# Kernel tuning notes

Hardware: AMD Instinct MI355X
Metric: run time of the kernel (lower is better)

Reference implementation:

```python
import jax, jax.numpy as jnp
import numpy as np

MAX_REL = 16  # max_relative_position (keys == values)


def _relative_positions(T, max_pos):
    r = jnp.arange(T)
    dist = r[None, :] - r[:, None]          # [T, T], k - q
    return jnp.clip(dist, -max_pos, max_pos) + max_pos


def setup_inputs() -> dict:
    key = jax.random.key(0)
    ks = jax.random.split(key, 5)
    B, H, T, D = 4, 16, 1024, 64
    V = 2 * MAX_REL + 1
    return {
        "q": jax.random.normal(ks[0], (B, H, T, D), jnp.float32),
        "k": jax.random.normal(ks[1], (B, H, T, D), jnp.float32),
        "v": jax.random.normal(ks[2], (B, H, T, D), jnp.float32),
        "emb_k": jax.random.normal(ks[3], (V, D), jnp.float32),
        "emb_v": jax.random.normal(ks[4], (V, D), jnp.float32),
    }


def reference(q, k, v, emb_k, emb_v):
    # q,k,v: [B,H,T,D]; emb_*: [2*MAX_REL+1, D]
    T = q.shape[2]
    D = k.shape[-1]
    rel_idx = _relative_positions(T, MAX_REL)          # [T,T]
    rel_k = emb_k[rel_idx]                             # [T,T,D]
    rel_v = emb_v[rel_idx]                             # [T,T,D]

    # content-content + content-position logits
    logits = jnp.einsum('bhtd,bhsd->bhts', q, k)
    logits = logits + jnp.einsum('bhtd,tsd->bhts', q, rel_k)
    logits = logits * (1.0 / jnp.sqrt(jnp.float32(D)))

    attn = jax.nn.softmax(logits, axis=-1)             # [B,H,T,T]
    out = jnp.einsum('bhts,bhsd->bhtd', attn, v)
    out = out + jnp.einsum('bhts,tsd->bhtd', attn, rel_v)
    return out, attn
```

## Files before the change

kernel.cpp:

```cpp
#include <hip/hip_runtime.h>
#include <hip/hip_bf16.h>

#define TT 1024
#define DD 64
#define MAXREL 16
#define NV 33
#define QBLK 16
#define SCALE 0.125f
#define BH 64

typedef short bf16x8 __attribute__((ext_vector_type(8)));
typedef short bf16x4 __attribute__((ext_vector_type(4)));
typedef float f32x4 __attribute__((ext_vector_type(4)));

#define SBAR() __builtin_amdgcn_sched_barrier(0)
#define WAITV(N)   __builtin_amdgcn_s_waitcnt(0x0F70 | (N))
#define WAITLGKM() __builtin_amdgcn_s_waitcnt(0xC07F)

static __device__ inline void gload16(const void* g, void* l) {
    __builtin_amdgcn_global_load_lds(
        (const __attribute__((address_space(1))) void*)g,
        (__attribute__((address_space(3))) void*)l, 16, 0, 0);
}

static __device__ inline short f2bf(float f) {
    __hip_bfloat16 h = __float2bfloat16(f);
    return *(short*)&h;
}
static __device__ inline float bf2f(short s) {
    union { unsigned u; float f; } x;
    x.u = ((unsigned)(unsigned short)s) << 16;
    return x.f;
}
static __device__ inline bf16x8 pack8(float4 a, float4 b) {
    bf16x8 r;
    r[0]=f2bf(a.x); r[1]=f2bf(a.y); r[2]=f2bf(a.z); r[3]=f2bf(a.w);
    r[4]=f2bf(b.x); r[5]=f2bf(b.y); r[6]=f2bf(b.z); r[7]=f2bf(b.w);
    return r;
}

__global__ __launch_bounds__(256)
void prep_kernel(const float* __restrict__ k, const float* __restrict__ v,
                 short* __restrict__ kbuf, short* __restrict__ vt) {
    __shared__ short tile[64][66];
    const int bh = blockIdx.x >> 4;
    const int s0 = (blockIdx.x & 15) * 64;
    const int t  = threadIdx.x;
    const int r  = t >> 2;
    const int g  = t & 3;

    {
        const float* kp = k + ((size_t)bh * TT + s0 + r) * DD + g * 16;
        float4 a0 = *(const float4*)(kp);
        float4 a1 = *(const float4*)(kp + 4);
        float4 a2 = *(const float4*)(kp + 8);
        float4 a3 = *(const float4*)(kp + 12);
        short* dp = kbuf + ((size_t)bh * TT + s0 + r) * DD + g * 16;
        *(bf16x8*)dp       = pack8(a0, a1);
        *(bf16x8*)(dp + 8) = pack8(a2, a3);
    }
    {
        const float* vp = v + ((size_t)bh * TT + s0 + r) * DD + g * 16;
        float4 a0 = *(const float4*)(vp);
        float4 a1 = *(const float4*)(vp + 4);
        float4 a2 = *(const float4*)(vp + 8);
        float4 a3 = *(const float4*)(vp + 12);
        bf16x8 b0 = pack8(a0, a1), b1 = pack8(a2, a3);
        #pragma unroll
        for (int j = 0; j < 8; ++j) {
            tile[g * 16 + j][r]     = b0[j];
            tile[g * 16 + 8 + j][r] = b1[j];
        }
    }
    __syncthreads();
    {
        const int d = t >> 2, c = t & 3;
        bf16x8 o0 = *(const bf16x8*)&tile[d][c * 16];
        bf16x8 o1 = *(const bf16x8*)&tile[d][c * 16 + 8];
        short* dp = vt + ((size_t)bh * DD + d) * TT + s0 + c * 16;
        *(bf16x8*)dp       = o0;
        *(bf16x8*)(dp + 8) = o1;
    }
}

__global__ __launch_bounds__(512)
void relattn_kernel(const float* __restrict__ q_g,
                    const short* __restrict__ kb,
                    const short* __restrict__ vt,
                    const float* __restrict__ ek_g,
                    const float* __restrict__ ev_g,
                    float* __restrict__ out_g,
                    float* __restrict__ attn_g) {
    __shared__ __align__(16) char pbuf[QBLK * 2048];
    __shared__ __align__(16) char kstage[8 * 4096];
    __shared__ float pair_lds[4][16][16];
    __shared__ float qe_lds[QBLK * NV];
    __shared__ float w_lds[QBLK * NV];
    __shared__ float psum_lds[QBLK][8];
    __shared__ float psuf_lds[QBLK][8];
    __shared__ float pmid_lds[QBLK][8];
    __shared__ float inv_lds[QBLK];

    const int t    = threadIdx.x;
    const int bid  = blockIdx.x;
    const int wg   = ((bid & 7) << 9) | (bid >> 3);
    const int bh   = wg >> 6;
    const int q0   = (wg & 63) * QBLK;
    const int w    = t >> 6;
    const int lane = t & 63;
    const int lr   = lane & 15;
    const int akg  = lane >> 4;
    const int srl  = lane >> 3;
    const int sqg  = (lane & 7) ^ srl;

    const short* kgbase = kb + (size_t)bh * TT * DD;
    char* kst = kstage + w * 4096;

    auto KSTAGE = [&](int B, int NT) {
        const int s0 = w * 128 + NT * 16;
        gload16(kgbase + (size_t)(s0 + srl) * 64 + sqg * 8,     kst + B * 2048);
        gload16(kgbase + (size_t)(s0 + 8 + srl) * 64 + sqg * 8, kst + B * 2048 + 1024);
    };

    bf16x8 qF0, qF1;
    {
        const float* qp = q_g + ((size_t)bh * TT + q0 + lr) * DD + akg * 8;
        float4 a = *(const float4*)qp,        b = *(const float4*)(qp + 4);
        float4 c = *(const float4*)(qp + 32), d = *(const float4*)(qp + 36);
        qF0 = pack8(a, b); qF1 = pack8(c, d);
    }

    KSTAGE(0, 0); KSTAGE(1, 1);

    for (int i = t; i < QBLK * NV; i += 512) w_lds[i] = 0.f;
    if (w < 3) {
        int v = w * 16 + lr; if (v > 32) v = 32;
        const float* ep = ek_g + v * DD + akg * 8;
        float4 a = *(const float4*)ep,        b = *(const float4*)(ep + 4);
        float4 c = *(const float4*)(ep + 32), d = *(const float4*)(ep + 36);
        bf16x8 eF0 = pack8(a, b), eF1 = pack8(c, d);
        f32x4 qacc = {0.f, 0.f, 0.f, 0.f};
        qacc = __builtin_amdgcn_mfma_f32_16x16x32_bf16(eF0, qF0, qacc, 0, 0, 0);
        qacc = __builtin_amdgcn_mfma_f32_16x16x32_bf16(eF1, qF1, qacc, 0, 0, 0);
        #pragma unroll
        for (int j = 0; j < 4; ++j) {
            int vv = w * 16 + akg * 4 + j;
            if (vv < NV) qe_lds[lr * NV + vv] = __expf(qacc[j] * SCALE);
        }
    }
    __syncthreads();

    {
        const int tq = q0 + lr;
        const int X  = (lr & 7) << 4;
        const float eqe_lo = qe_lds[lr * NV];
        const float eqe_hi = qe_lds[lr * NV + 32];
        float sum = 0.f, suff = 0.f, msum = 0.f;

        auto CVALU = [&](f32x4 acc, int nt) {
            const int sb = w * 128 + nt * 16 + akg * 4;
            float ex0 = __expf(acc[0] * SCALE), ex1 = __expf(acc[1] * SCALE);
            float ex2 = __expf(acc[2] * SCALE), ex3 = __expf(acc[3] * SCALE);
            float e0, e1, e2, e3;
            if (sb >= tq + MAXREL) {
                e0 = ex0 * eqe_hi; e1 = ex1 * eqe_hi;
                e2 = ex2 * eqe_hi; e3 = ex3 * eqe_hi;
                float csum = (e0 + e1) + (e2 + e3);
                sum += csum; suff += csum;
            } else if (sb + 3 <= tq - MAXREL) {
                e0 = ex0 * eqe_lo; e1 = ex1 * eqe_lo;
                e2 = ex2 * eqe_lo; e3 = ex3 * eqe_lo;
                sum += (e0 + e1) + (e2 + e3);
            } else {
                float ee[4]; float exs[4] = {ex0, ex1, ex2, ex3};
                #pragma unroll
                for (int j = 0; j < 4; ++j) {
                    int dr = sb + j - tq;
                    int dc = dr < -MAXREL ? -MAXREL : (dr > MAXREL ? MAXREL : dr);
                    float v = exs[j] * qe_lds[lr * NV + dc + MAXREL];
                    ee[j] = v;
                    sum += v;
                    if (dr >= MAXREL) suff += v;
                    if (dr > -MAXREL && dr < MAXREL) {
                        w_lds[lr * NV + dr + MAXREL] = v;
                        msum += v;
                    }
                }
                e0 = ee[0]; e1 = ee[1]; e2 = ee[2]; e3 = ee[3];
            }
            bf16x4 p4;
            p4[0] = f2bf(e0); p4[1] = f2bf(e1);
            p4[2] = f2bf(e2); p4[3] = f2bf(e3);
            *(bf16x4*)(pbuf + lr * 2048 + ((2 * sb) ^ X)) = p4;
        };

        auto MFMA2 = [&](bf16x8 kf0, bf16x8 kf1) {
            f32x4 acc = {0.f, 0.f, 0.f, 0.f};
            acc = __builtin_amdgcn_mfma_f32_16x16x32_bf16(kf0, qF0, acc, 0, 0, 0);
            acc = __builtin_amdgcn_mfma_f32_16x16x32_bf16(kf1, qF1, acc, 0, 0, 0);
            return acc;
        };

        f32x4 aA, aB;
        #define CITER(B, NT, W, PF, AC, AP, NP) \
            WAITV(W); SBAR(); \
            { bf16x8 kf0 = *(const bf16x8*)(kst + (B)*2048 + lr*128 + ((((akg))  ^(lr&7)) << 4)); \
              bf16x8 kf1 = *(const bf16x8*)(kst + (B)*2048 + lr*128 + ((((akg)+4)^(lr&7)) << 4)); \
              if ((NP) >= 0) CVALU(AP, NP); \
              WAITLGKM(); SBAR(); \
              if (PF) KSTAGE((B), (NT) + 2); \
              AC = MFMA2(kf0, kf1); } \
            SBAR()
        CITER(0, 0, 2, 1, aA, aB, -1);
        CITER(1, 1, 2, 1, aB, aA,  0);
        CITER(0, 2, 2, 1, aA, aB,  1);
        CITER(1, 3, 2, 1, aB, aA,  2);
        CITER(0, 4, 2, 1, aA, aB,  3);
        CITER(1, 5, 2, 1, aB, aA,  4);
        CITER(0, 6, 2, 0, aA, aB,  5);
        CITER(1, 7, 0, 0, aB, aA,  6);
        CVALU(aB, 7);
        #undef CITER

        {
            WAITLGKM(); SBAR();
            const short* vgbase = vt + ((size_t)bh * DD + (w & 3) * 16) * TT;
            const int S0 = (w >> 2) * 8;
            gload16(vgbase + (size_t)srl * TT + S0 * 64 + sqg * 8,           kst);
            gload16(vgbase + (size_t)(8 + srl) * TT + S0 * 64 + sqg * 8,     kst + 1024);
            gload16(vgbase + (size_t)srl * TT + (S0 + 1) * 64 + sqg * 8,     kst + 2048);
            gload16(vgbase + (size_t)(8 + srl) * TT + (S0 + 1) * 64 + sqg * 8, kst + 3072);
        }

        sum  += __shfl_xor(sum, 16);  sum  += __shfl_xor(sum, 32);
        suff += __shfl_xor(suff, 16); suff += __shfl_xor(suff, 32);
        msum += __shfl_xor(msum, 16); msum += __shfl_xor(msum, 32);
        if (lane < 16) {
            psum_lds[lr][w] = sum;
            psuf_lds[lr][w] = suff;
            pmid_lds[lr][w] = msum;
        }
    }
    __syncthreads();

    if (t < QBLK) {
        float s = 0.f, sf = 0.f, sm = 0.f;
        #pragma unroll
        for (int i = 0; i < 8; ++i) {
            s  += psum_lds[t][i];
            sf += psuf_lds[t][i];
            sm += pmid_lds[t][i];
        }
        inv_lds[t] = 1.0f / s;
        w_lds[t * NV]      = s - sf - sm;
        w_lds[t * NV + 32] = sf;
    }
    __syncthreads();

    {
        const int dt = w & 3;
        const int sh = w >> 2;
        const int S0 = sh * 8;
        const int lc = lane & 15;
        const int dcol = dt * 16 + lc;
        const char* pb = pbuf + lc * 2048;
        const int X = (lc & 7) << 4;
        char* vst = kst;
        const short* vgbase = vt + ((size_t)bh * DD + dt * 16) * TT;
        float* ab = attn_g + ((size_t)bh * TT + q0) * TT;
        f32x4 acc0 = {0.f, 0.f, 0.f, 0.f};
        f32x4 acc1 = {0.f, 0.f, 0.f, 0.f};

        auto VSTAGE = [&](int B, int S) {
            gload16(vgbase + (size_t)srl * TT + S * 64 + sqg * 8,       vst + B * 2048);
            gload16(vgbase + (size_t)(8 + srl) * TT + S * 64 + sqg * 8, vst + B * 2048 + 1024);
        };

        auto ASTORE = [&](int ST) {
            const int r_ = w * 2 + (ST >> 2);
            const int i_ = ST & 3;
            const float inv_ = inv_lds[r_];
            const int Xr = (r_ & 7) << 4;
            bf16x4 p4 = *(const bf16x4*)(pbuf + r_ * 2048 + ((8 * lane + 512 * i_) ^ Xr));
            f32x4 o;
            o[0] = bf2f(p4[0]) * inv_; o[1] = bf2f(p4[1]) * inv_;
            o[2] = bf2f(p4[2]) * inv_; o[3] = bf2f(p4[3]) * inv_;
            __builtin_nontemporal_store(o, (f32x4*)(ab + (size_t)r_ * TT + lane * 4 + 256 * i_));
        };

        #define FITER(B, S, W, PF, AC, ST) \
            WAITV(W); SBAR(); \
            { ASTORE(ST); \
              bf16x8 vf0 = *(const bf16x8*)(vst + (B)*2048 + lc*128 + ((((akg))  ^(lc&7)) << 4)); \
              bf16x8 vf1 = *(const bf16x8*)(vst + (B)*2048 + lc*128 + ((((akg)+4)^(lc&7)) << 4)); \
              bf16x8 a0 = *(const bf16x8*)(pb + (((2*(S))*64     + akg*16) ^ X)); \
              bf16x8 a1 = *(const bf16x8*)(pb + (((2*(S)+1)*64   + akg*16) ^ X)); \
              WAITLGKM(); SBAR(); \
              if (PF) VSTAGE((B), (S) + 2); \
              AC = __builtin_amdgcn_mfma_f32_16x16x32_bf16(a0, vf0, AC, 0, 0, 0); \
              AC = __builtin_amdgcn_mfma_f32_16x16x32_bf16(a1, vf1, AC, 0, 0, 0); } \
            SBAR()
        FITER(0, S0 + 0, 2, 1, acc0, 0);  FITER(1, S0 + 1, 2, 1, acc1, 1);
        FITER(0, S0 + 2, 2, 1, acc0, 2);  FITER(1, S0 + 3, 2, 1, acc1, 3);
        FITER(0, S0 + 4, 2, 1, acc0, 4);  FITER(1, S0 + 5, 2, 1, acc1, 5);
        FITER(0, S0 + 6, 2, 0, acc0, 6);  FITER(1, S0 + 7, 0, 0, acc1, 7);
        #undef FITER

        f32x4 acc;
        acc[0] = acc0[0] + acc1[0]; acc[1] = acc0[1] + acc1[1];
        acc[2] = acc0[2] + acc1[2]; acc[3] = acc0[3] + acc1[3];

        if (sh == 1) {
            #pragma unroll
            for (int j = 0; j < 4; ++j)
                pair_lds[dt][akg * 4 + j][lc] = acc[j];
        }
        __syncthreads();

        if (sh == 0) {
            const int rb = akg * 4;
            float o0 = acc[0] + pair_lds[dt][rb + 0][lc];
            float o1 = acc[1] + pair_lds[dt][rb + 1][lc];
            float o2 = acc[2] + pair_lds[dt][rb + 2][lc];
            float o3 = acc[3] + pair_lds[dt][rb + 3][lc];
            #pragma unroll 8
            for (int v = 0; v < NV; ++v) {
                float ev = ev_g[v * DD + dcol];
                o0 += w_lds[(rb + 0) * NV + v] * ev;
                o1 += w_lds[(rb + 1) * NV + v] * ev;
                o2 += w_lds[(rb + 2) * NV + v] * ev;
                o3 += w_lds[(rb + 3) * NV + v] * ev;
            }
            float* op = out_g + ((size_t)bh * TT + q0 + rb) * DD + dcol;
            op[0 * DD] = o0 * inv_lds[rb + 0];
            op[1 * DD] = o1 * inv_lds[rb + 1];
            op[2 * DD] = o2 * inv_lds[rb + 2];
            op[3 * DD] = o3 * inv_lds[rb + 3];
        }
    }
}

extern "C" void kernel_launch(void* const* d_in, const int* in_sizes, int n_in,
                              void* d_out, int out_size, void* d_ws, size_t ws_size,
                              hipStream_t stream) {
    const float* q  = (const float*)d_in[0];
    const float* k  = (const float*)d_in[1];
    const float* v  = (const float*)d_in[2];
    const float* ek = (const float*)d_in[3];
    const float* ev = (const float*)d_in[4];
    float* out  = (float*)d_out;
    float* attn = out + (size_t)BH * TT * DD;

    short* kbuf = (short*)d_ws;
    short* vtb  = kbuf + (size_t)BH * TT * DD;

    prep_kernel<<<dim3(1024), dim3(256), 0, stream>>>(k, v, kbuf, vtb);
    relattn_kernel<<<dim3(4096), dim3(512), 0, stream>>>(q, kbuf, vtb, ek, ev, out, attn);
}
```

Measured before the change: 120.1 us.

## Spread QK tile loop over ten waves and store partial sums in bf16

The block grows from 8 to 10 waves, and the 64 key tiles of the QK/softmax phase are split unevenly: four waves take 7 tiles and six waves take 6. Each wave's serial pipelined loop gets shorter. The PV phase and the output epilogue stay on waves 0-7 and 0-3, so the two extra waves sit idle there. Per-wave partial softmax sums and the cross-wave PV pair reduction are now kept in LDS as bf16 instead of fp32, which loses accuracy in the normaliser and the output. The larger LDS footprint and 640-thread blocks may also lower occupancy.

```diff
diff --git a/kernel.cpp b/kernel.cpp
--- a/kernel.cpp
+++ b/kernel.cpp
@@ -8,6 +8,7 @@
 #define QBLK 16
 #define SCALE 0.125f
 #define BH 64
+#define NW 10
 
 typedef short bf16x8 __attribute__((ext_vector_type(8)));
 typedef short bf16x4 __attribute__((ext_vector_type(4)));
@@ -48,7 +49,6 @@
     const int t  = threadIdx.x;
     const int r  = t >> 2;
     const int g  = t & 3;
-
     {
         const float* kp = k + ((size_t)bh * TT + s0 + r) * DD + g * 16;
         float4 a0 = *(const float4*)(kp);
@@ -83,7 +83,7 @@
     }
 }
 
-__global__ __launch_bounds__(512)
+__global__ __launch_bounds__(640)
 void relattn_kernel(const float* __restrict__ q_g,
                     const short* __restrict__ kb,
                     const short* __restrict__ vt,
@@ -92,13 +92,13 @@
                     float* __restrict__ out_g,
                     float* __restrict__ attn_g) {
     __shared__ __align__(16) char pbuf[QBLK * 2048];
-    __shared__ __align__(16) char kstage[8 * 4096];
-    __shared__ float pair_lds[4][16][16];
+    __shared__ __align__(16) char kstage[NW * 4096];
+    __shared__ short pair_lds[4][16][16];
     __shared__ float qe_lds[QBLK * NV];
     __shared__ float w_lds[QBLK * NV];
-    __shared__ float psum_lds[QBLK][8];
-    __shared__ float psuf_lds[QBLK][8];
-    __shared__ float pmid_lds[QBLK][8];
+    __shared__ short psum_lds[QBLK][NW];
+    __shared__ short psuf_lds[QBLK][NW];
+    __shared__ short pmid_lds[QBLK][NW];
     __shared__ float inv_lds[QBLK];
 
     const int t    = threadIdx.x;
@@ -113,11 +113,15 @@
     const int srl  = lane >> 3;
     const int sqg  = (lane & 7) ^ srl;
 
+    const int start = (w < 4) ? (7 * w) : (28 + 6 * (w - 4));
+    const bool real7 = (w < 4);
+
     const short* kgbase = kb + (size_t)bh * TT * DD;
     char* kst = kstage + w * 4096;
 
-    auto KSTAGE = [&](int B, int NT) {
-        const int s0 = w * 128 + NT * 16;
+    auto KSTAGE = [&](int B, int TILE) {
+        const int tc = TILE > 63 ? 63 : TILE;
+        const int s0 = tc * 16;
         gload16(kgbase + (size_t)(s0 + srl) * 64 + sqg * 8,     kst + B * 2048);
         gload16(kgbase + (size_t)(s0 + 8 + srl) * 64 + sqg * 8, kst + B * 2048 + 1024);
     };
@@ -130,9 +134,9 @@
         qF0 = pack8(a, b); qF1 = pack8(c, d);
     }
 
-    KSTAGE(0, 0); KSTAGE(1, 1);
-
-    for (int i = t; i < QBLK * NV; i += 512) w_lds[i] = 0.f;
+    KSTAGE(0, start); KSTAGE(1, start + 1);
+
+    for (int i = t; i < QBLK * NV; i += 640) w_lds[i] = 0.f;
     if (w < 3) {
         int v = w * 16 + lr; if (v > 32) v = 32;
         const float* ep = ek_g + v * DD + akg * 8;
@@ -157,8 +161,8 @@
         const float eqe_hi = qe_lds[lr * NV + 32];
         float sum = 0.f, suff = 0.f, msum = 0.f;
 
-        auto CVALU = [&](f32x4 acc, int nt) {
-            const int sb = w * 128 + nt * 16 + akg * 4;
+        auto CVALU = [&](f32x4 acc, int TILE) {
+            const int sb = TILE * 16 + akg * 4;
             float ex0 = __expf(acc[0] * SCALE), ex1 = __expf(acc[1] * SCALE);
             float ex2 = __expf(acc[2] * SCALE), ex3 = __expf(acc[3] * SCALE);
             float e0, e1, e2, e3;
@@ -206,9 +210,9 @@
             WAITV(W); SBAR(); \
             { bf16x8 kf0 = *(const bf16x8*)(kst + (B)*2048 + lr*128 + ((((akg))  ^(lr&7)) << 4)); \
               bf16x8 kf1 = *(const bf16x8*)(kst + (B)*2048 + lr*128 + ((((akg)+4)^(lr&7)) << 4)); \
-              if ((NP) >= 0) CVALU(AP, NP); \
+              if ((NP) >= 0) CVALU(AP, start + (NP)); \
               WAITLGKM(); SBAR(); \
-              if (PF) KSTAGE((B), (NT) + 2); \
+              if (PF) KSTAGE((B), start + (NT) + 2); \
               AC = MFMA2(kf0, kf1); } \
             SBAR()
         CITER(0, 0, 2, 1, aA, aB, -1);
@@ -216,13 +220,12 @@
         CITER(0, 2, 2, 1, aA, aB,  1);
         CITER(1, 3, 2, 1, aB, aA,  2);
         CITER(0, 4, 2, 1, aA, aB,  3);
-        CITER(1, 5, 2, 1, aB, aA,  4);
-        CITER(0, 6, 2, 0, aA, aB,  5);
-        CITER(1, 7, 0, 0, aB, aA,  6);
-        CVALU(aB, 7);
+        CITER(1, 5, 2, 0, aB, aA,  4);
+        CITER(0, 6, 0, 0, aA, aB,  5);
+        if (real7) CVALU(aA, start + 6);
         #undef CITER
 
-        {
+        if (w < 8) {
             WAITLGKM(); SBAR();
             const short* vgbase = vt + ((size_t)bh * DD + (w & 3) * 16) * TT;
             const int S0 = (w >> 2) * 8;
@@ -236,9 +239,9 @@
         suff += __shfl_xor(suff, 16); suff += __shfl_xor(suff, 32);
         msum += __shfl_xor(msum, 16); msum += __shfl_xor(msum, 32);
         if (lane < 16) {
-            psum_lds[lr][w] = sum;
-            psuf_lds[lr][w] = suff;
-            pmid_lds[lr][w] = msum;
+            psum_lds[lr][w] = f2bf(sum);
+            psuf_lds[lr][w] = f2bf(suff);
+            pmid_lds[lr][w] = f2bf(msum);
         }
     }
     __syncthreads();
@@ -246,10 +249,10 @@
     if (t < QBLK) {
         float s = 0.f, sf = 0.f, sm = 0.f;
         #pragma unroll
-        for (int i = 0; i < 8; ++i) {
-            s  += psum_lds[t][i];
-            sf += psuf_lds[t][i];
-            sm += pmid_lds[t][i];
+        for (int i = 0; i < NW; ++i) {
+            s  += bf2f(psum_lds[t][i]);
+            sf += bf2f(psuf_lds[t][i]);
+            sm += bf2f(pmid_lds[t][i]);
         }
         inv_lds[t] = 1.0f / s;
         w_lds[t * NV]      = s - sf - sm;
@@ -257,12 +260,12 @@
     }
     __syncthreads();
 
-    {
+    f32x4 facc = {0.f, 0.f, 0.f, 0.f};
+    if (w < 8) {
         const int dt = w & 3;
         const int sh = w >> 2;
         const int S0 = sh * 8;
         const int lc = lane & 15;
-        const int dcol = dt * 16 + lc;
         const char* pb = pbuf + lc * 2048;
         const int X = (lc & 7) << 4;
         char* vst = kst;
@@ -306,37 +309,40 @@
         FITER(0, S0 + 6, 2, 0, acc0, 6);  FITER(1, S0 + 7, 0, 0, acc1, 7);
         #undef FITER
 
-        f32x4 acc;
-        acc[0] = acc0[0] + acc1[0]; acc[1] = acc0[1] + acc1[1];
-        acc[2] = acc0[2] + acc1[2]; acc[3] = acc0[3] + acc1[3];
+        facc[0] = acc0[0] + acc1[0]; facc[1] = acc0[1] + acc1[1];
+        facc[2] = acc0[2] + acc1[2]; facc[3] = acc0[3] + acc1[3];
 
         if (sh == 1) {
+            const int lc2 = lane & 15;
             #pragma unroll
             for (int j = 0; j < 4; ++j)
-                pair_lds[dt][akg * 4 + j][lc] = acc[j];
-        }
-        __syncthreads();
-
-        if (sh == 0) {
-            const int rb = akg * 4;
-            float o0 = acc[0] + pair_lds[dt][rb + 0][lc];
-            float o1 = acc[1] + pair_lds[dt][rb + 1][lc];
-            float o2 = acc[2] + pair_lds[dt][rb + 2][lc];
-            float o3 = acc[3] + pair_lds[dt][rb + 3][lc];
-            #pragma unroll 8
-            for (int v = 0; v < NV; ++v) {
-                float ev = ev_g[v * DD + dcol];
-                o0 += w_lds[(rb + 0) * NV + v] * ev;
-                o1 += w_lds[(rb + 1) * NV + v] * ev;
-                o2 += w_lds[(rb + 2) * NV + v] * ev;
-                o3 += w_lds[(rb + 3) * NV + v] * ev;
-            }
-            float* op = out_g + ((size_t)bh * TT + q0 + rb) * DD + dcol;
-            op[0 * DD] = o0 * inv_lds[rb + 0];
-            op[1 * DD] = o1 * inv_lds[rb + 1];
-            op[2 * DD] = o2 * inv_lds[rb + 2];
-            op[3 * DD] = o3 * inv_lds[rb + 3];
-        }
+                pair_lds[dt][akg * 4 + j][lc2] = f2bf(facc[j]);
+        }
+    }
+    __syncthreads();
+
+    if (w < 4) {
+        const int dt = w & 3;
+        const int lc = lane & 15;
+        const int dcol = dt * 16 + lc;
+        const int rb = akg * 4;
+        float o0 = facc[0] + bf2f(pair_lds[dt][rb + 0][lc]);
+        float o1 = facc[1] + bf2f(pair_lds[dt][rb + 1][lc]);
+        float o2 = facc[2] + bf2f(pair_lds[dt][rb + 2][lc]);
+        float o3 = facc[3] + bf2f(pair_lds[dt][rb + 3][lc]);
+        #pragma unroll 8
+        for (int v = 0; v < NV; ++v) {
+            float ev = ev_g[v * DD + dcol];
+            o0 += w_lds[(rb + 0) * NV + v] * ev;
+            o1 += w_lds[(rb + 1) * NV + v] * ev;
+            o2 += w_lds[(rb + 2) * NV + v] * ev;
+            o3 += w_lds[(rb + 3) * NV + v] * ev;
+        }
+        float* op = out_g + ((size_t)bh * TT + q0 + rb) * DD + dcol;
+        op[0 * DD] = o0 * inv_lds[rb + 0];
+        op[1 * DD] = o1 * inv_lds[rb + 1];
+        op[2 * DD] = o2 * inv_lds[rb + 2];
+        op[3 * DD] = o3 * inv_lds[rb + 3];
     }
 }
 
@@ -355,5 +361,5 @@
     short* vtb  = kbuf + (size_t)BH * TT * DD;
 
     prep_kernel<<<dim3(1024), dim3(256), 0, stream>>>(k, v, kbuf, vtb);
-    relattn_kernel<<<dim3(4096), dim3(512), 0, stream>>>(q, kbuf, vtb, ek, ev, out, attn);
-}
+    relattn_kernel<<<dim3(4096), dim3(640), 0, stream>>>(q, kbuf, vtb, ek, ev, out, attn);
+}
```

Measured after the change: 145.1 us. 1.21x slower.
